# Optimization experiments

Hardware: AMD Instinct MI355X
Metric: run time of the kernel (lower is better)

The kernel has to match this reference:

```python
import jax, jax.numpy as jnp
import numpy as np
import math

F = 64        # num_features (multiplicity of each irrep)
N = 16000     # nodes
E = 256000    # edges (avg_num_neighbors = 16)
S = 4         # num_species
DE = 32       # scalar edge feature dim (radial basis)
W = 128       # interaction_mlp_width
AVG_NEIGH = 16.0
SQ2 = math.sqrt(2.0)
SQ3 = math.sqrt(3.0)


def setup_inputs() -> dict:
    key = jax.random.key(0)
    ks = jax.random.split(key, 32)
    def nrm(k, shape, scale=1.0):
        return jax.random.normal(k, shape, dtype=jnp.float32) * scale
    inp = {}
    # forward args
    inp["vectors"] = nrm(ks[0], (E, 1, 3))
    inp["lengths"] = jax.random.uniform(ks[1], (E, 1), dtype=jnp.float32)
    inp["node_s"] = nrm(ks[2], (N, F))            # 64x0e part of node_feats
    inp["node_v"] = nrm(ks[3], (N, F, 3))         # 64x1o part of node_feats
    inp["scalar_edge_feats"] = nrm(ks[4], (E, DE))
    inp["node_specie"] = jax.random.randint(ks[5], (N,), 0, S)
    inp["senders"] = jax.random.randint(ks[6], (E,), 0, N)
    inp["receivers"] = jax.random.randint(ks[7], (E,), 0, N)
    # parameters (e3nn Linear = per-irrep channel mixing, fan-in normalized; bias only on 0e)
    inp["W_up_s"] = nrm(ks[8], (F, F), F ** -0.5); inp["b_up_s"] = jnp.zeros((F,), jnp.float32)
    inp["W_up_v"] = nrm(ks[9], (F, F), F ** -0.5)
    din = 2 * F + DE + 1
    inp["mlp_W1"] = nrm(ks[10], (din, W), din ** -0.5); inp["mlp_b1"] = jnp.zeros((W,), jnp.float32)
    inp["mlp_W2"] = nrm(ks[11], (W, W), W ** -0.5); inp["mlp_b2"] = jnp.zeros((W,), jnp.float32)
    inp["mlp_W3"] = nrm(ks[12], (W, 3 * F), W ** -0.5); inp["mlp_b3"] = jnp.zeros((3 * F,), jnp.float32)
    inp["W_dn_s"] = nrm(ks[13], (F, F), F ** -0.5); inp["b_dn_s"] = jnp.zeros((F,), jnp.float32)
    inp["W_dn_v"] = nrm(ks[14], (2 * F, F), (2 * F) ** -0.5)
    # symmetric contraction weights (per species, per channel); correlation=2
    inp["w_sc_s"] = nrm(ks[15], (S, 3, F), 3 ** -0.5)   # paths to 0e: x0, x0^2, (x1.x1)/sqrt3
    inp["w_sc_v"] = nrm(ks[16], (S, 2, F), 2 ** -0.5)   # paths to 1o: x1, x0*x1
    inp["W_pb_s"] = nrm(ks[17], (F, F), F ** -0.5); inp["b_pb_s"] = jnp.zeros((F,), jnp.float32)
    inp["W_pb_v"] = nrm(ks[18], (F, F), F ** -0.5)
    inp["W_r1_s"] = nrm(ks[19], (F, 2 * F), F ** -0.5); inp["b_r1_s"] = jnp.zeros((2 * F,), jnp.float32)
    inp["W_r1_v"] = nrm(ks[20], (F, F), F ** -0.5)
    inp["W_r2_s"] = nrm(ks[21], (F, 1), F ** -0.5); inp["b_r2"] = jnp.zeros((1,), jnp.float32)
    inp["W_r2_v"] = nrm(ks[22], (F, 1), F ** -0.5)
    return inp


def reference(vectors, lengths, node_s, node_v, scalar_edge_feats, node_specie,
              senders, receivers,
              W_up_s, b_up_s, W_up_v,
              mlp_W1, mlp_b1, mlp_W2, mlp_b2, mlp_W3, mlp_b3,
              W_dn_s, b_dn_s, W_dn_v,
              w_sc_s, w_sc_v, W_pb_s, b_pb_s, W_pb_v,
              W_r1_s, b_r1_s, W_r1_v, W_r2_s, b_r2, W_r2_v):
    n = node_s.shape[0]
    # --- spherical harmonics, sh_irreps='1o', component normalization, normalize=False ---
    edge_v = SQ3 * vectors[:, 0, :]                              # [E,3]

    # --- InteractionBlock: linear_up ---
    h_s = node_s @ W_up_s + b_up_s                               # [N,F]
    h_v = jnp.einsum('nfi,fg->ngi', node_v, W_up_v)              # [N,F,3]

    # --- MessagePassingConvolution ---
    m_s = h_s[senders]                                           # [E,F] 0e
    m_v = h_v[senders]                                           # [E,F,3] 1o
    # tensor product with edge 1o, filtered to 0e+1o (unitary CG):
    tp_s = jnp.einsum('efi,ei->ef', m_v, edge_v) / SQ3           # 1o x 1o -> 0e  [E,F]
    tp_v1 = m_s[:, :, None] * edge_v[:, None, :]                 # 0e x 1o -> 1o  [E,F,3]
    tp_v2 = jnp.cross(m_v, edge_v[:, None, :]) / SQ2             # 1o x 1o -> 1o  [E,F,3]
    # scalar MLP mix (one scalar weight per output irrep = 3F)
    mlp_in = jnp.concatenate([m_s, h_s[receivers], scalar_edge_feats, lengths], axis=1)
    h = jax.nn.silu(mlp_in @ mlp_W1 + mlp_b1)
    h = jax.nn.silu(h @ mlp_W2 + mlp_b2)
    mix = h @ mlp_W3 + mlp_b3                                    # [E,3F]
    mix_s, mix_v1, mix_v2 = mix[:, :F], mix[:, F:2 * F], mix[:, 2 * F:]
    tp_s = tp_s * mix_s
    tp_v = jnp.concatenate([tp_v1 * mix_v1[:, :, None], tp_v2 * mix_v2[:, :, None]], axis=1)  # [E,2F,3]
    # scatter-add to receivers, normalize by avg_num_neighbors
    agg_s = jax.ops.segment_sum(tp_s, receivers, num_segments=n) / AVG_NEIGH   # [N,F]
    agg_v = jax.ops.segment_sum(tp_v, receivers, num_segments=n) / AVG_NEIGH   # [N,2F,3]
    # linear_down
    f_s = agg_s @ W_dn_s + b_dn_s                                # [N,F]
    f_v = jnp.einsum('nfi,fg->ngi', agg_v, W_dn_v)               # [N,F,3]

    # --- EquivariantProductBasisBlock: symmetric contraction (correlation=2), per-species ---
    ws = w_sc_s[node_specie]                                     # [N,3,F]
    wv = w_sc_v[node_specie]                                     # [N,2,F]
    vv = jnp.sum(f_v * f_v, axis=-1) / SQ3                       # 1o (x) 1o -> 0e, symmetric
    sc_s = ws[:, 0] * f_s + ws[:, 1] * (f_s * f_s) + ws[:, 2] * vv           # [N,F]
    sc_v = wv[:, 0][:, :, None] * f_v + wv[:, 1][:, :, None] * (f_s[:, :, None] * f_v)  # [N,F,3]
    p_s = sc_s @ W_pb_s + b_pb_s                                 # node_feats 0e out
    p_v = jnp.einsum('nfi,fg->ngi', sc_v, W_pb_v)                # node_feats 1o out

    # --- NonLinearReadoutBlock: linear to (2F x 0e + F x 1o), gate, linear to 1x0e+1x1o ---
    r_s = p_s @ W_r1_s + b_r1_s                                  # [N,2F]
    r_v = jnp.einsum('nfi,fg->ngi', p_v, W_r1_v)                 # [N,F,3]
    act = jax.nn.silu(r_s[:, :F])
    gates = jax.nn.silu(r_s[:, F:])
    g_v = gates[:, :, None] * r_v                                # gated vectors
    out_s = act @ W_r2_s + b_r2                                  # [N,1]  0e output
    out_v = jnp.einsum('nfi,fo->noi', g_v, W_r2_v)               # [N,1,3] 1o output
    return out_s, out_v, p_s, p_v
```

## Files before the change

kernel.cpp:

```cpp
#include <hip/hip_runtime.h>

typedef short bf16x8 __attribute__((ext_vector_type(8)));
typedef float f32x4  __attribute__((ext_vector_type(4)));
typedef unsigned short ushort_t;

__device__ __forceinline__ float silu(float x) {
    float t = __expf(-x);
    return x * __builtin_amdgcn_rcpf(1.f + t);
}

__device__ __forceinline__ ushort_t f2bs(float x) {
    union { float f; unsigned int u; } v; v.f = x;
    unsigned int r = v.u + 0x7FFF + ((v.u >> 16) & 1);
    return (ushort_t)(r >> 16);
}
__device__ __forceinline__ ushort_t f2bs_t(float x) {
    union { float f; unsigned int u; } v; v.f = x;
    return (ushort_t)(v.u >> 16);
}
__device__ __forceinline__ float bs2f(ushort_t x) {
    union { unsigned int u; float f; } v; v.u = ((unsigned int)x) << 16; return v.f;
}

constexpr int N_   = 16000;
constexpr int E_   = 256000;
constexpr int Fd   = 64;

constexpr float SQ3f    = 1.7320508075688772f;
constexpr float INV_SQ3 = 0.5773502691896258f;
constexpr float INV_SQ2 = 0.7071067811865476f;
constexpr float INV_AVG = 0.0625f;

constexpr int OFF_OS = 0;
constexpr int OFF_OV = N_;
constexpr int OFF_PS = OFF_OV + 3 * N_;
constexpr int OFF_PV = OFF_PS + N_ * Fd;

constexpr int W1P_SZ = 6 * 8 * 512;
constexpr int W2P_SZ = 4 * 8 * 512;
constexpr int W3P_SZ = 4 * 12 * 512;

__global__ __launch_bounds__(256) void pack_kernel(
    const float* __restrict__ W1, const float* __restrict__ W2,
    const float* __restrict__ W3,
    ushort_t* __restrict__ W1p, ushort_t* __restrict__ W2p,
    ushort_t* __restrict__ W3p)
{
    int idx = blockIdx.x * 256 + threadIdx.x;
    if (idx < W1P_SZ) {
        int j = idx & 7, lane = (idx >> 3) & 63, tile = idx >> 9;
        int c = tile >> 3, t = tile & 7;
        int k = c * 32 + (lane >> 4) * 8 + j;
        int n = t * 16 + (lane & 15);
        W1p[idx] = f2bs(k < 161 ? W1[k * 128 + n] : 0.f);
    } else if (idx < W1P_SZ + W2P_SZ) {
        int q = idx - W1P_SZ;
        int j = q & 7, lane = (q >> 3) & 63, tile = q >> 9;
        int c = tile >> 3, t = tile & 7;
        int k = c * 32 + (lane >> 4) * 8 + j;
        int n = t * 16 + (lane & 15);
        W2p[q] = f2bs(W2[k * 128 + n]);
    } else {
        int q = idx - W1P_SZ - W2P_SZ;
        int j = q & 7, lane = (q >> 3) & 63, tile = q >> 9;
        int c = tile / 12, t = tile % 12;
        int k = c * 32 + (lane >> 4) * 8 + j;
        int n = t * 16 + (lane & 15);
        W3p[q] = f2bs(W3[k * 192 + n]);
    }
}

__global__ __launch_bounds__(64, 4) void up_kernel(
    const float* __restrict__ node_s, const float* __restrict__ node_v,
    const float* __restrict__ W_up_s, const float* __restrict__ b_up_s,
    const float* __restrict__ W_up_v,
    const int* __restrict__ receivers, int* __restrict__ cnt,
    ushort_t* __restrict__ hs_bf, float* __restrict__ h_v)
{
    __shared__ float ns[4][64];
    __shared__ float nv[4][64][3];
    const int n0 = blockIdx.x * 4;
    const int g  = threadIdx.x;

    {
        int e = blockIdx.x * 64 + g;
        atomicAdd(&cnt[receivers[e]], 1);
    }

    #pragma unroll
    for (int j = 0; j < 4; j++) ns[j][g] = node_s[(n0 + j) * 64 + g];
    for (int idx = g; idx < 4 * 192; idx += 64) {
        int j = idx / 192, r = idx - j * 192;
        nv[j][r / 3][r % 3] = node_v[(size_t)n0 * 192 + idx];
    }
    __syncthreads();

    float as[4], a0[4], a1[4], a2[4];
    float bb = b_up_s[g];
    #pragma unroll
    for (int j = 0; j < 4; j++) { as[j] = bb; a0[j] = a1[j] = a2[j] = 0.f; }
    #pragma unroll 4
    for (int f = 0; f < 64; f++) {
        float wss = W_up_s[f * 64 + g];
        float wv  = W_up_v[f * 64 + g];
        #pragma unroll
        for (int j = 0; j < 4; j++) {
            as[j] += ns[j][f] * wss;
            a0[j] += nv[j][f][0] * wv;
            a1[j] += nv[j][f][1] * wv;
            a2[j] += nv[j][f][2] * wv;
        }
    }
    #pragma unroll
    for (int j = 0; j < 4; j++) {
        hs_bf[(n0 + j) * 64 + g] = f2bs(as[j]);
        h_v[(n0 + j) * 192 + 0 * 64 + g] = a0[j];
        h_v[(n0 + j) * 192 + 1 * 64 + g] = a1[j];
        h_v[(n0 + j) * 192 + 2 * 64 + g] = a2[j];
    }
}

__global__ __launch_bounds__(1024) void scan_kernel(
    const int* __restrict__ cnt, int* __restrict__ base, int* __restrict__ cursor)
{
    __shared__ int part[1024];
    const int t = threadIdx.x;
    int v[16];
    int s = 0;
    if (t < 1000) {
        const int4* c4 = (const int4*)(cnt + t * 16);
        #pragma unroll
        for (int q = 0; q < 4; q++) {
            int4 w = c4[q];
            v[q * 4 + 0] = w.x; v[q * 4 + 1] = w.y;
            v[q * 4 + 2] = w.z; v[q * 4 + 3] = w.w;
            s += w.x + w.y + w.z + w.w;
        }
    }
    part[t] = s;
    __syncthreads();
    for (int off = 1; off < 1024; off <<= 1) {
        int u = (t >= off) ? part[t - off] : 0;
        __syncthreads();
        part[t] += u;
        __syncthreads();
    }
    if (t < 1000) {
        int run = part[t] - s;
        int b[16];
        #pragma unroll
        for (int i = 0; i < 16; i++) { b[i] = run; run += v[i]; }
        int4* bb = (int4*)(base + t * 16);
        int4* cc = (int4*)(cursor + t * 16);
        #pragma unroll
        for (int q = 0; q < 4; q++) {
            int4 w = { b[q * 4], b[q * 4 + 1], b[q * 4 + 2], b[q * 4 + 3] };
            bb[q] = w;
            cc[q] = w;
        }
    }
}

__global__ __launch_bounds__(256, 3) void edge_mlp_kernel(
    const float* __restrict__ lengths, const float* __restrict__ sef,
    const int* __restrict__ senders, const int* __restrict__ receivers,
    const float* __restrict__ vectors,
    const float* __restrict__ b1f, const float* __restrict__ b2f,
    const float* __restrict__ b3f,
    const ushort_t* __restrict__ hs_bf,
    const ushort_t* __restrict__ W1p, const ushort_t* __restrict__ W2p,
    const ushort_t* __restrict__ W3p,
    int* __restrict__ cursor, float4* __restrict__ meta,
    ushort_t* __restrict__ tpx)
{
    __shared__ ushort_t Als[64 * 200];
    __shared__ ushort_t Hs[64 * 136];
    __shared__ int perm_s[64];

    const int tid  = threadIdx.x;
    const int wave = tid >> 6, lane = tid & 63;
    const int quad = lane >> 4, l4 = lane & 15;
    const int e0   = blockIdx.x * 64;

    if (tid < 64) {
        int e = e0 + tid;
        int p = atomicAdd(&cursor[receivers[e]], 1);
        perm_s[tid] = p;
        float4 mt;
        mt.x = __int_as_float(senders[e]);
        mt.y = SQ3f * vectors[e * 3 + 0];
        mt.z = SQ3f * vectors[e * 3 + 1];
        mt.w = SQ3f * vectors[e * 3 + 2];
        meta[p] = mt;
    }

    {
        const int e  = tid & 63;
        const int ge = e0 + e;
        const int snd = senders[ge];
        const int rcv = receivers[ge];
        for (int c = tid >> 6; c < 24; c += 4) {
            bf16x8 v;
            if (c < 8) {
                v = *(const bf16x8*)(hs_bf + snd * 64 + c * 8);
            } else if (c < 16) {
                v = *(const bf16x8*)(hs_bf + rcv * 64 + (c - 8) * 8);
            } else if (c < 20) {
                const float4 s0 = *(const float4*)(sef + (size_t)ge * 32 + (c - 16) * 8);
                const float4 s1 = *(const float4*)(sef + (size_t)ge * 32 + (c - 16) * 8 + 4);
                v[0] = (short)f2bs(s0.x); v[1] = (short)f2bs(s0.y);
                v[2] = (short)f2bs(s0.z); v[3] = (short)f2bs(s0.w);
                v[4] = (short)f2bs(s1.x); v[5] = (short)f2bs(s1.y);
                v[6] = (short)f2bs(s1.z); v[7] = (short)f2bs(s1.w);
            } else if (c == 20) {
                v = (bf16x8){0,0,0,0,0,0,0,0};
                v[0] = (short)f2bs(lengths[ge]);
            } else {
                v = (bf16x8){0,0,0,0,0,0,0,0};
            }
            *(bf16x8*)(&Als[e * 200 + c * 8]) = v;
        }
    }
    __syncthreads();

    const bf16x8* B1 = (const bf16x8*)W1p;
    const bf16x8* B2 = (const bf16x8*)W2p;
    const bf16x8* B3 = (const bf16x8*)W3p;

    {
        f32x4 acc[2][4];
        #pragma unroll
        for (int ti = 0; ti < 2; ti++)
            #pragma unroll
            for (int m = 0; m < 4; m++) acc[ti][m] = (f32x4){0,0,0,0};
        #pragma unroll
        for (int c = 0; c < 6; c++) {
            bf16x8 b0 = B1[(c * 8 + wave * 2 + 0) * 64 + lane];
            bf16x8 b1 = B1[(c * 8 + wave * 2 + 1) * 64 + lane];
            #pragma unroll
            for (int m = 0; m < 4; m++) {
                bf16x8 a = *(const bf16x8*)(&Als[(m * 16 + l4) * 200 + c * 32 + quad * 8]);
                acc[0][m] = __builtin_amdgcn_mfma_f32_16x16x32_bf16(a, b0, acc[0][m], 0, 0, 0);
                acc[1][m] = __builtin_amdgcn_mfma_f32_16x16x32_bf16(a, b1, acc[1][m], 0, 0, 0);
            }
        }
        #pragma unroll
        for (int ti = 0; ti < 2; ti++) {
            int t = wave * 2 + ti;
            float bb = b1f[t * 16 + l4];
            #pragma unroll
            for (int m = 0; m < 4; m++)
                #pragma unroll
                for (int r = 0; r < 4; r++)
                    Hs[(m * 16 + quad * 4 + r) * 136 + t * 16 + l4] =
                        f2bs_t(silu(acc[ti][m][r] + bb));
        }
    }
    __syncthreads();

    {
        f32x4 acc[2][4];
        #pragma unroll
        for (int ti = 0; ti < 2; ti++)
            #pragma unroll
            for (int m = 0; m < 4; m++) acc[ti][m] = (f32x4){0,0,0,0};
        #pragma unroll
        for (int c = 0; c < 4; c++) {
            bf16x8 b0 = B2[(c * 8 + wave * 2 + 0) * 64 + lane];
            bf16x8 b1 = B2[(c * 8 + wave * 2 + 1) * 64 + lane];
            #pragma unroll
            for (int m = 0; m < 4; m++) {
                bf16x8 a = *(const bf16x8*)(&Hs[(m * 16 + l4) * 136 + c * 32 + quad * 8]);
                acc[0][m] = __builtin_amdgcn_mfma_f32_16x16x32_bf16(a, b0, acc[0][m], 0, 0, 0);
                acc[1][m] = __builtin_amdgcn_mfma_f32_16x16x32_bf16(a, b1, acc[1][m], 0, 0, 0);
            }
        }
        #pragma unroll
        for (int ti = 0; ti < 2; ti++) {
            int t = wave * 2 + ti;
            float bb = b2f[t * 16 + l4];
            #pragma unroll
            for (int m = 0; m < 4; m++)
                #pragma unroll
                for (int r = 0; r < 4; r++)
                    Als[(m * 16 + quad * 4 + r) * 136 + t * 16 + l4] =
                        f2bs_t(silu(acc[ti][m][r] + bb));
        }
    }
    __syncthreads();

    {
        f32x4 acc[3][4];
        #pragma unroll
        for (int ti = 0; ti < 3; ti++)
            #pragma unroll
            for (int m = 0; m < 4; m++) acc[ti][m] = (f32x4){0,0,0,0};
        #pragma unroll
        for (int c = 0; c < 4; c++) {
            bf16x8 b0 = B3[(c * 12 + wave * 3 + 0) * 64 + lane];
            bf16x8 b1 = B3[(c * 12 + wave * 3 + 1) * 64 + lane];
            bf16x8 b2 = B3[(c * 12 + wave * 3 + 2) * 64 + lane];
            #pragma unroll
            for (int m = 0; m < 4; m++) {
                bf16x8 a = *(const bf16x8*)(&Als[(m * 16 + l4) * 136 + c * 32 + quad * 8]);
                acc[0][m] = __builtin_amdgcn_mfma_f32_16x16x32_bf16(a, b0, acc[0][m], 0, 0, 0);
                acc[1][m] = __builtin_amdgcn_mfma_f32_16x16x32_bf16(a, b1, acc[1][m], 0, 0, 0);
                acc[2][m] = __builtin_amdgcn_mfma_f32_16x16x32_bf16(a, b2, acc[2][m], 0, 0, 0);
            }
        }
        #pragma unroll
        for (int ti = 0; ti < 3; ti++) {
            int t = wave * 3 + ti;
            float bb = b3f[t * 16 + l4];
            #pragma unroll
            for (int m = 0; m < 4; m++)
                #pragma unroll
                for (int r = 0; r < 4; r++) {
                    int p = perm_s[m * 16 + quad * 4 + r];
                    tpx[(size_t)p * 192 + t * 16 + l4] = f2bs(acc[ti][m][r] + bb);
                }
        }
    }
}

__global__ __launch_bounds__(256, 2) void node_fused_kernel(
    const int* __restrict__ base, const int* __restrict__ cnt,
    const float4* __restrict__ meta,
    const ushort_t* __restrict__ tpx,
    const ushort_t* __restrict__ hs_bf, const float* __restrict__ h_v,
    const int* __restrict__ specie,
    const float* __restrict__ W_dn_s, const float* __restrict__ b_dn_s,
    const float* __restrict__ W_dn_v,
    const float* __restrict__ w_sc_s, const float* __restrict__ w_sc_v,
    const float* __restrict__ W_pb_s, const float* __restrict__ b_pb_s,
    const float* __restrict__ W_pb_v,
    const float* __restrict__ W_r1_s, const float* __restrict__ b_r1_s,
    const float* __restrict__ W_r1_v,
    const float* __restrict__ W_r2_s, const float* __restrict__ b_r2,
    const float* __restrict__ W_r2_v,
    float* __restrict__ out)
{
    __shared__ float as_l[4][64];
    __shared__ float av_l[4][128][3];
    __shared__ float scs[4][64];
    __shared__ float scv[4][64][3];
    __shared__ float ps_[4][64];
    __shared__ float pv_[4][64][3];
    __shared__ float4 lmeta[4][64];

    const int tid = threadIdx.x;
    const int w   = tid >> 6;
    const int g   = tid & 63;
    const int n   = blockIdx.x * 4 + w;

    const int b = base[n];
    const int c = cnt[n];
    float accSa = 0.f, accSb = 0.f;
    float a10a = 0.f, a11a = 0.f, a12a = 0.f;
    float a20a = 0.f, a21a = 0.f, a22a = 0.f;
    float a10b = 0.f, a11b = 0.f, a12b = 0.f;
    float a20b = 0.f, a21b = 0.f, a22b = 0.f;

    for (int done = 0; done < c; done += 64) {
        int m = min(64, c - done);
        if (g < m) lmeta[w][g] = meta[b + done + g];
        int i = 0;
        for (; i + 1 < m; i += 2) {
            const float4 mt1 = lmeta[w][i];
            const float4 mt2 = lmeta[w][i + 1];
            const int se1 = __float_as_int(mt1.x);
            const int se2 = __float_as_int(mt2.x);
            const float ev10 = mt1.y, ev11 = mt1.z, ev12 = mt1.w;
            const float ev20 = mt2.y, ev21 = mt2.z, ev22 = mt2.w;
            const float m10 = h_v[(size_t)se1 * 192 + 0 * 64 + g];
            const float m11 = h_v[(size_t)se1 * 192 + 1 * 64 + g];
            const float m12 = h_v[(size_t)se1 * 192 + 2 * 64 + g];
            const float m20 = h_v[(size_t)se2 * 192 + 0 * 64 + g];
            const float m21 = h_v[(size_t)se2 * 192 + 1 * 64 + g];
            const float m22 = h_v[(size_t)se2 * 192 + 2 * 64 + g];
            const float ms1 = bs2f(hs_bf[se1 * 64 + g]);
            const float ms2 = bs2f(hs_bf[se2 * 64 + g]);
            const ushort_t* r1 = tpx + (size_t)(b + done + i) * 192;
            const ushort_t* r2 = r1 + 192;
            const float c10 = bs2f(r1[g]), c11 = bs2f(r1[64 + g]), c12 = bs2f(r1[128 + g]);
            const float c20 = bs2f(r2[g]), c21 = bs2f(r2[64 + g]), c22 = bs2f(r2[128 + g]);

            accSa += (m10 * ev10 + m11 * ev11 + m12 * ev12) * c10;
            accSb += (m20 * ev20 + m21 * ev21 + m22 * ev22) * c20;
            float k1a = ms1 * c11, k1b = ms2 * c21;
            a10a += k1a * ev10; a11a += k1a * ev11; a12a += k1a * ev12;
            a10b += k1b * ev20; a11b += k1b * ev21; a12b += k1b * ev22;
            a20a += (m11 * ev12 - m12 * ev11) * c12;
            a21a += (m12 * ev10 - m10 * ev12) * c12;
            a22a += (m10 * ev11 - m11 * ev10) * c12;
            a20b += (m21 * ev22 - m22 * ev21) * c22;
            a21b += (m22 * ev20 - m20 * ev22) * c22;
            a22b += (m20 * ev21 - m21 * ev20) * c22;
        }
        if (i < m) {
            const float4 mt1 = lmeta[w][i];
            const int se1 = __float_as_int(mt1.x);
            const float ev10 = mt1.y, ev11 = mt1.z, ev12 = mt1.w;
            const float m10 = h_v[(size_t)se1 * 192 + 0 * 64 + g];
            const float m11 = h_v[(size_t)se1 * 192 + 1 * 64 + g];
            const float m12 = h_v[(size_t)se1 * 192 + 2 * 64 + g];
            const float ms1 = bs2f(hs_bf[se1 * 64 + g]);
            const ushort_t* r1 = tpx + (size_t)(b + done + i) * 192;
            const float c10 = bs2f(r1[g]), c11 = bs2f(r1[64 + g]), c12 = bs2f(r1[128 + g]);
            accSa += (m10 * ev10 + m11 * ev11 + m12 * ev12) * c10;
            float k1a = ms1 * c11;
            a10a += k1a * ev10; a11a += k1a * ev11; a12a += k1a * ev12;
            a20a += (m11 * ev12 - m12 * ev11) * c12;
            a21a += (m12 * ev10 - m10 * ev12) * c12;
            a22a += (m10 * ev11 - m11 * ev10) * c12;
        }
    }
    as_l[w][g] = (accSa + accSb) * (INV_SQ3 * INV_AVG);
    av_l[w][g][0] = (a10a + a10b) * INV_AVG;
    av_l[w][g][1] = (a11a + a11b) * INV_AVG;
    av_l[w][g][2] = (a12a + a12b) * INV_AVG;
    av_l[w][64 + g][0] = (a20a + a20b) * (INV_SQ2 * INV_AVG);
    av_l[w][64 + g][1] = (a21a + a21b) * (INV_SQ2 * INV_AVG);
    av_l[w][64 + g][2] = (a22a + a22b) * (INV_SQ2 * INV_AVG);

    float f_s = b_dn_s[g];
    #pragma unroll 8
    for (int f = 0; f < 64; f++) f_s += as_l[w][f] * W_dn_s[f * 64 + g];
    float fv0 = 0.f, fv1 = 0.f, fv2 = 0.f;
    #pragma unroll 8
    for (int f = 0; f < 128; f++) {
        float wt = W_dn_v[f * 64 + g];
        fv0 += av_l[w][f][0] * wt;
        fv1 += av_l[w][f][1] * wt;
        fv2 += av_l[w][f][2] * wt;
    }

    float vv = (fv0 * fv0 + fv1 * fv1 + fv2 * fv2) * INV_SQ3;
    int sp = specie[n];
    float ws0 = w_sc_s[sp * 192 + 0 * 64 + g];
    float ws1 = w_sc_s[sp * 192 + 1 * 64 + g];
    float ws2 = w_sc_s[sp * 192 + 2 * 64 + g];
    float wv0 = w_sc_v[sp * 128 + 0 * 64 + g];
    float wv1 = w_sc_v[sp * 128 + 1 * 64 + g];
    float sc_s = ws0 * f_s + ws1 * f_s * f_s + ws2 * vv;
    float kv = wv0 + wv1 * f_s;
    scs[w][g] = sc_s;
    scv[w][g][0] = kv * fv0;
    scv[w][g][1] = kv * fv1;
    scv[w][g][2] = kv * fv2;

    float p_s = b_pb_s[g];
    float pv0 = 0.f, pv1 = 0.f, pv2 = 0.f;
    #pragma unroll 8
    for (int f = 0; f < 64; f++) {
        float wps = W_pb_s[f * 64 + g];
        p_s += scs[w][f] * wps;
        float wpv = W_pb_v[f * 64 + g];
        pv0 += scv[w][f][0] * wpv;
        pv1 += scv[w][f][1] * wpv;
        pv2 += scv[w][f][2] * wpv;
    }
    ps_[w][g] = p_s;
    pv_[w][g][0] = pv0; pv_[w][g][1] = pv1; pv_[w][g][2] = pv2;

    out[OFF_PS + n * 64 + g] = p_s;
    out[OFF_PV + (size_t)n * 192 + g * 3 + 0] = pv0;
    out[OFF_PV + (size_t)n * 192 + g * 3 + 1] = pv1;
    out[OFF_PV + (size_t)n * 192 + g * 3 + 2] = pv2;

    float r0 = b_r1_s[g];
    float r1 = b_r1_s[g + 64];
    float rv0 = 0.f, rv1 = 0.f, rv2 = 0.f;
    #pragma unroll 8
    for (int f = 0; f < 64; f++) {
        float p = ps_[w][f];
        r0 += p * W_r1_s[f * 128 + g];
        r1 += p * W_r1_s[f * 128 + g + 64];
        float wrv = W_r1_v[f * 64 + g];
        rv0 += pv_[w][f][0] * wrv;
        rv1 += pv_[w][f][1] * wrv;
        rv2 += pv_[w][f][2] * wrv;
    }
    float act  = silu(r0);
    float gate = silu(r1);
    float o_s = act * W_r2_s[g];
    float wr2v = W_r2_v[g];
    float ov0 = gate * rv0 * wr2v;
    float ov1 = gate * rv1 * wr2v;
    float ov2 = gate * rv2 * wr2v;

    #pragma unroll
    for (int off = 32; off > 0; off >>= 1) {
        o_s += __shfl_down(o_s, off);
        ov0 += __shfl_down(ov0, off);
        ov1 += __shfl_down(ov1, off);
        ov2 += __shfl_down(ov2, off);
    }
    if (g == 0) {
        out[OFF_OS + n] = o_s + b_r2[0];
        out[OFF_OV + n * 3 + 0] = ov0;
        out[OFF_OV + n * 3 + 1] = ov1;
        out[OFF_OV + n * 3 + 2] = ov2;
    }
}

extern "C" void kernel_launch(void* const* d_in, const int* in_sizes, int n_in,
                              void* d_out, int out_size, void* d_ws, size_t ws_size,
                              hipStream_t stream)
{
    const float* vectors  = (const float*)d_in[0];
    const float* lengths  = (const float*)d_in[1];
    const float* node_s   = (const float*)d_in[2];
    const float* node_v   = (const float*)d_in[3];
    const float* sef      = (const float*)d_in[4];
    const int*  specie    = (const int*)d_in[5];
    const int*  senders   = (const int*)d_in[6];
    const int*  receivers = (const int*)d_in[7];
    const float* W_up_s   = (const float*)d_in[8];
    const float* b_up_s   = (const float*)d_in[9];
    const float* W_up_v   = (const float*)d_in[10];
    const float* mlp_W1   = (const float*)d_in[11];
    const float* mlp_b1   = (const float*)d_in[12];
    const float* mlp_W2   = (const float*)d_in[13];
    const float* mlp_b2   = (const float*)d_in[14];
    const float* mlp_W3   = (const float*)d_in[15];
    const float* mlp_b3   = (const float*)d_in[16];
    const float* W_dn_s   = (const float*)d_in[17];
    const float* b_dn_s   = (const float*)d_in[18];
    const float* W_dn_v   = (const float*)d_in[19];
    const float* w_sc_s   = (const float*)d_in[20];
    const float* w_sc_v   = (const float*)d_in[21];
    const float* W_pb_s   = (const float*)d_in[22];
    const float* b_pb_s   = (const float*)d_in[23];
    const float* W_pb_v   = (const float*)d_in[24];
    const float* W_r1_s   = (const float*)d_in[25];
    const float* b_r1_s   = (const float*)d_in[26];
    const float* W_r1_v   = (const float*)d_in[27];
    const float* W_r2_s   = (const float*)d_in[28];
    const float* b_r2     = (const float*)d_in[29];
    const float* W_r2_v   = (const float*)d_in[30];

    float* h_v = (float*)d_ws;
    ushort_t* tpx   = (ushort_t*)(h_v + (size_t)N_ * 192);
    ushort_t* hs_bf = tpx + (size_t)E_ * 192;
    ushort_t* W1p   = hs_bf + (size_t)N_ * 64;
    ushort_t* W2p   = W1p + W1P_SZ;
    ushort_t* W3p   = W2p + W2P_SZ;
    float4* meta    = (float4*)((((size_t)(W3p + W3P_SZ)) + 15) & ~(size_t)15);
    int* cnt        = (int*)(meta + E_);
    int* base       = cnt + N_;
    int* cursor     = base + N_;

    float* out = (float*)d_out;

    hipMemsetAsync(cnt, 0, N_ * sizeof(int), stream);

    up_kernel<<<N_ / 4, 64, 0, stream>>>(node_s, node_v, W_up_s, b_up_s, W_up_v,
                                         receivers, cnt, hs_bf, h_v);
    pack_kernel<<<256, 256, 0, stream>>>(mlp_W1, mlp_W2, mlp_W3, W1p, W2p, W3p);
    scan_kernel<<<1, 1024, 0, stream>>>(cnt, base, cursor);

    edge_mlp_kernel<<<E_ / 64, 256, 0, stream>>>(
        lengths, sef, senders, receivers, vectors,
        mlp_b1, mlp_b2, mlp_b3,
        hs_bf, W1p, W2p, W3p, cursor, meta, tpx);

    node_fused_kernel<<<N_ / 4, 256, 0, stream>>>(
        base, cnt, meta,
        tpx, hs_bf, h_v, specie,
        W_dn_s, b_dn_s, W_dn_v, w_sc_s, w_sc_v,
        W_pb_s, b_pb_s, W_pb_v, W_r1_s, b_r1_s, W_r1_v,
        W_r2_s, b_r2, W_r2_v, out);
}
```

Measured before the change: 367.1 us.

## Compute per-edge tensor-product messages in edge kernel, store fp16 contributions

The edge MLP kernel now gathers sender node features and computes the full per-edge tensor-product contributions (scalar, vector and cross-product paths). It writes them as fp16 rows in receiver-sorted order. The node kernel then only sums these precomputed rows plus a small edge-vector term, so it no longer does random gathers of sender features. The cost is more bytes written and read per edge (320 fp16 values instead of 192 bf16 values) and an extra LDS staging pass and barrier in the edge kernel. Using fp16 for the contributions also changes precision.

New measurement: 389.0 us. +5.9%, slower.

```diff
diff --git a/kernel.cpp b/kernel.cpp
--- a/kernel.cpp
+++ b/kernel.cpp
@@ -3,6 +3,7 @@
 typedef short bf16x8 __attribute__((ext_vector_type(8)));
 typedef float f32x4  __attribute__((ext_vector_type(4)));
 typedef unsigned short ushort_t;
+typedef _Float16 half_t;
 
 __device__ __forceinline__ float silu(float x) {
     float t = __expf(-x);
@@ -39,6 +40,8 @@
 constexpr int W1P_SZ = 6 * 8 * 512;
 constexpr int W2P_SZ = 4 * 8 * 512;
 constexpr int W3P_SZ = 4 * 12 * 512;
+
+constexpr int CTR_W = 320;
 
 __global__ __launch_bounds__(256) void pack_kernel(
     const float* __restrict__ W1, const float* __restrict__ W2,
@@ -167,15 +170,17 @@
     const float* __restrict__ vectors,
     const float* __restrict__ b1f, const float* __restrict__ b2f,
     const float* __restrict__ b3f,
-    const ushort_t* __restrict__ hs_bf,
+    const ushort_t* __restrict__ hs_bf, const float* __restrict__ h_v,
     const ushort_t* __restrict__ W1p, const ushort_t* __restrict__ W2p,
     const ushort_t* __restrict__ W3p,
-    int* __restrict__ cursor, float4* __restrict__ meta,
-    ushort_t* __restrict__ tpx)
+    int* __restrict__ cursor, float4* __restrict__ evx,
+    half_t* __restrict__ ctr)
 {
     __shared__ ushort_t Als[64 * 200];
     __shared__ ushort_t Hs[64 * 136];
     __shared__ int perm_s[64];
+    __shared__ int snd_s[64];
+    __shared__ float ev_s[64][3];
 
     const int tid  = threadIdx.x;
     const int wave = tid >> 6, lane = tid & 63;
@@ -186,12 +191,13 @@
         int e = e0 + tid;
         int p = atomicAdd(&cursor[receivers[e]], 1);
         perm_s[tid] = p;
-        float4 mt;
-        mt.x = __int_as_float(senders[e]);
-        mt.y = SQ3f * vectors[e * 3 + 0];
-        mt.z = SQ3f * vectors[e * 3 + 1];
-        mt.w = SQ3f * vectors[e * 3 + 2];
-        meta[p] = mt;
+        snd_s[tid] = senders[e];
+        float v0 = SQ3f * vectors[e * 3 + 0];
+        float v1 = SQ3f * vectors[e * 3 + 1];
+        float v2 = SQ3f * vectors[e * 3 + 2];
+        ev_s[tid][0] = v0; ev_s[tid][1] = v1; ev_s[tid][2] = v2;
+        float4 mt; mt.x = v0; mt.y = v1; mt.z = v2; mt.w = 0.f;
+        evx[p] = mt;
     }
 
     {
@@ -308,6 +314,7 @@
                 acc[2][m] = __builtin_amdgcn_mfma_f32_16x16x32_bf16(a, b2, acc[2][m], 0, 0, 0);
             }
         }
+        __syncthreads();
         #pragma unroll
         for (int ti = 0; ti < 3; ti++) {
             int t = wave * 3 + ti;
@@ -315,19 +322,42 @@
             #pragma unroll
             for (int m = 0; m < 4; m++)
                 #pragma unroll
-                for (int r = 0; r < 4; r++) {
-                    int p = perm_s[m * 16 + quad * 4 + r];
-                    tpx[(size_t)p * 192 + t * 16 + l4] = f2bs(acc[ti][m][r] + bb);
-                }
+                for (int r = 0; r < 4; r++)
+                    Als[(m * 16 + quad * 4 + r) * 200 + t * 16 + l4] =
+                        f2bs(acc[ti][m][r] + bb);
+        }
+    }
+    __syncthreads();
+
+    {
+        const int g = lane;
+        #pragma unroll 4
+        for (int j = 0; j < 16; j++) {
+            const int el = wave * 16 + j;
+            const int se = snd_s[el];
+            const int p  = perm_s[el];
+            const float ev0 = ev_s[el][0], ev1 = ev_s[el][1], ev2 = ev_s[el][2];
+            const float m0 = h_v[(size_t)se * 192 + 0 * 64 + g];
+            const float m1 = h_v[(size_t)se * 192 + 1 * 64 + g];
+            const float m2 = h_v[(size_t)se * 192 + 2 * 64 + g];
+            const float ms = bs2f(hs_bf[se * 64 + g]);
+            const float mixs  = bs2f(Als[el * 200 +   0 + g]);
+            const float mixv1 = bs2f(Als[el * 200 +  64 + g]);
+            const float mixv2 = bs2f(Als[el * 200 + 128 + g]);
+            half_t* row = ctr + (size_t)p * CTR_W;
+            row[  0 + g] = (half_t)((m0 * ev0 + m1 * ev1 + m2 * ev2) * mixs);
+            row[ 64 + g] = (half_t)(ms * mixv1);
+            row[128 + g] = (half_t)((m1 * ev2 - m2 * ev1) * mixv2);
+            row[192 + g] = (half_t)((m2 * ev0 - m0 * ev2) * mixv2);
+            row[256 + g] = (half_t)((m0 * ev1 - m1 * ev0) * mixv2);
         }
     }
 }
 
 __global__ __launch_bounds__(256, 2) void node_fused_kernel(
     const int* __restrict__ base, const int* __restrict__ cnt,
-    const float4* __restrict__ meta,
-    const ushort_t* __restrict__ tpx,
-    const ushort_t* __restrict__ hs_bf, const float* __restrict__ h_v,
+    const float4* __restrict__ evx,
+    const half_t* __restrict__ ctr,
     const int* __restrict__ specie,
     const float* __restrict__ W_dn_s, const float* __restrict__ b_dn_s,
     const float* __restrict__ W_dn_v,
@@ -363,56 +393,40 @@
 
     for (int done = 0; done < c; done += 64) {
         int m = min(64, c - done);
-        if (g < m) lmeta[w][g] = meta[b + done + g];
+        if (g < m) lmeta[w][g] = evx[b + done + g];
         int i = 0;
         for (; i + 1 < m; i += 2) {
-            const float4 mt1 = lmeta[w][i];
-            const float4 mt2 = lmeta[w][i + 1];
-            const int se1 = __float_as_int(mt1.x);
-            const int se2 = __float_as_int(mt2.x);
-            const float ev10 = mt1.y, ev11 = mt1.z, ev12 = mt1.w;
-            const float ev20 = mt2.y, ev21 = mt2.z, ev22 = mt2.w;
-            const float m10 = h_v[(size_t)se1 * 192 + 0 * 64 + g];
-            const float m11 = h_v[(size_t)se1 * 192 + 1 * 64 + g];
-            const float m12 = h_v[(size_t)se1 * 192 + 2 * 64 + g];
-            const float m20 = h_v[(size_t)se2 * 192 + 0 * 64 + g];
-            const float m21 = h_v[(size_t)se2 * 192 + 1 * 64 + g];
-            const float m22 = h_v[(size_t)se2 * 192 + 2 * 64 + g];
-            const float ms1 = bs2f(hs_bf[se1 * 64 + g]);
-            const float ms2 = bs2f(hs_bf[se2 * 64 + g]);
-            const ushort_t* r1 = tpx + (size_t)(b + done + i) * 192;
-            const ushort_t* r2 = r1 + 192;
-            const float c10 = bs2f(r1[g]), c11 = bs2f(r1[64 + g]), c12 = bs2f(r1[128 + g]);
-            const float c20 = bs2f(r2[g]), c21 = bs2f(r2[64 + g]), c22 = bs2f(r2[128 + g]);
-
-            accSa += (m10 * ev10 + m11 * ev11 + m12 * ev12) * c10;
-            accSb += (m20 * ev20 + m21 * ev21 + m22 * ev22) * c20;
-            float k1a = ms1 * c11, k1b = ms2 * c21;
-            a10a += k1a * ev10; a11a += k1a * ev11; a12a += k1a * ev12;
-            a10b += k1b * ev20; a11b += k1b * ev21; a12b += k1b * ev22;
-            a20a += (m11 * ev12 - m12 * ev11) * c12;
-            a21a += (m12 * ev10 - m10 * ev12) * c12;
-            a22a += (m10 * ev11 - m11 * ev10) * c12;
-            a20b += (m21 * ev22 - m22 * ev21) * c22;
-            a21b += (m22 * ev20 - m20 * ev22) * c22;
-            a22b += (m20 * ev21 - m21 * ev20) * c22;
+            const float4 t1 = lmeta[w][i];
+            const float4 t2 = lmeta[w][i + 1];
+            const half_t* r1 = ctr + (size_t)(b + done + i) * CTR_W;
+            const half_t* r2 = r1 + CTR_W;
+            const float cs1 = (float)r1[g];
+            const float k1  = (float)r1[64 + g];
+            const float c10 = (float)r1[128 + g];
+            const float c11 = (float)r1[192 + g];
+            const float c12 = (float)r1[256 + g];
+            const float cs2 = (float)r2[g];
+            const float k2  = (float)r2[64 + g];
+            const float c20 = (float)r2[128 + g];
+            const float c21 = (float)r2[192 + g];
+            const float c22 = (float)r2[256 + g];
+
+            accSa += cs1; accSb += cs2;
+            a10a += k1 * t1.x; a11a += k1 * t1.y; a12a += k1 * t1.z;
+            a10b += k2 * t2.x; a11b += k2 * t2.y; a12b += k2 * t2.z;
+            a20a += c10; a21a += c11; a22a += c12;
+            a20b += c20; a21b += c21; a22b += c22;
         }
         if (i < m) {
-            const float4 mt1 = lmeta[w][i];
-            const int se1 = __float_as_int(mt1.x);
-            const float ev10 = mt1.y, ev11 = mt1.z, ev12 = mt1.w;
-            const float m10 = h_v[(size_t)se1 * 192 + 0 * 64 + g];
-            const float m11 = h_v[(size_t)se1 * 192 + 1 * 64 + g];
-            const float m12 = h_v[(size_t)se1 * 192 + 2 * 64 + g];
-            const float ms1 = bs2f(hs_bf[se1 * 64 + g]);
-            const ushort_t* r1 = tpx + (size_t)(b + done + i) * 192;
-            const float c10 = bs2f(r1[g]), c11 = bs2f(r1[64 + g]), c12 = bs2f(r1[128 + g]);
-            accSa += (m10 * ev10 + m11 * ev11 + m12 * ev12) * c10;
-            float k1a = ms1 * c11;
-            a10a += k1a * ev10; a11a += k1a * ev11; a12a += k1a * ev12;
-            a20a += (m11 * ev12 - m12 * ev11) * c12;
-            a21a += (m12 * ev10 - m10 * ev12) * c12;
-            a22a += (m10 * ev11 - m11 * ev10) * c12;
+            const float4 t1 = lmeta[w][i];
+            const half_t* r1 = ctr + (size_t)(b + done + i) * CTR_W;
+            const float cs1 = (float)r1[g];
+            const float k1  = (float)r1[64 + g];
+            accSa += cs1;
+            a10a += k1 * t1.x; a11a += k1 * t1.y; a12a += k1 * t1.z;
+            a20a += (float)r1[128 + g];
+            a21a += (float)r1[192 + g];
+            a22a += (float)r1[256 + g];
         }
     }
     as_l[w][g] = (accSa + accSb) * (INV_SQ3 * INV_AVG);
@@ -541,13 +555,13 @@
     const float* W_r2_v   = (const float*)d_in[30];
 
     float* h_v = (float*)d_ws;
-    ushort_t* tpx   = (ushort_t*)(h_v + (size_t)N_ * 192);
-    ushort_t* hs_bf = tpx + (size_t)E_ * 192;
+    half_t* ctr = (half_t*)(h_v + (size_t)N_ * 192);
+    ushort_t* hs_bf = (ushort_t*)(ctr + (size_t)E_ * CTR_W);
     ushort_t* W1p   = hs_bf + (size_t)N_ * 64;
     ushort_t* W2p   = W1p + W1P_SZ;
     ushort_t* W3p   = W2p + W2P_SZ;
-    float4* meta    = (float4*)((((size_t)(W3p + W3P_SZ)) + 15) & ~(size_t)15);
-    int* cnt        = (int*)(meta + E_);
+    float4* evx     = (float4*)((((size_t)(W3p + W3P_SZ)) + 15) & ~(size_t)15);
+    int* cnt        = (int*)(evx + E_);
     int* base       = cnt + N_;
     int* cursor     = base + N_;
 
@@ -563,11 +577,11 @@
     edge_mlp_kernel<<<E_ / 64, 256, 0, stream>>>(
         lengths, sef, senders, receivers, vectors,
         mlp_b1, mlp_b2, mlp_b3,
-        hs_bf, W1p, W2p, W3p, cursor, meta, tpx);
+        hs_bf, h_v, W1p, W2p, W3p, cursor, evx, ctr);
 
     node_fused_kernel<<<N_ / 4, 256, 0, stream>>>(
-        base, cnt, meta,
-        tpx, hs_bf, h_v, specie,
+        base, cnt, evx,
+        ctr, specie,
         W_dn_s, b_dn_s, W_dn_v, w_sc_s, w_sc_v,
         W_pb_s, b_pb_s, W_pb_v, W_r1_s, b_r1_s, W_r1_v,
         W_r2_s, b_r2, W_r2_v, out);
```
